# Performance work log

Hardware: AMD Instinct MI355X
Metric: run time of the kernel (lower is better)

## Reference

```python
import jax, jax.numpy as jnp
import numpy as np

HEADS = 16
DIM_HEAD = 64
SCALE = DIM_HEAD ** -0.5


def setup_inputs() -> dict:
    key = jax.random.key(0)
    ks = jax.random.split(key, 6)
    d = 1024
    x = jax.random.normal(ks[0], (4, 2048, d), dtype=jnp.float32)
    s = d ** -0.5
    Wq = jax.random.normal(ks[1], (d, d), dtype=jnp.float32) * s
    Wk = jax.random.normal(ks[2], (d, d), dtype=jnp.float32) * s
    Wv = jax.random.normal(ks[3], (d, d), dtype=jnp.float32) * s
    Wo = jax.random.normal(ks[4], (d, d), dtype=jnp.float32) * s
    bo = jnp.zeros((d,), dtype=jnp.float32)
    return {"x": x, "Wq": Wq, "Wk": Wk, "Wv": Wv, "Wo": Wo, "bo": bo}


def reference(x, Wq, Wk, Wv, Wo, bo):
    b, n, _ = x.shape
    h, dh = HEADS, DIM_HEAD
    # projections (bias-free), split heads: b n (h d) -> b h n d
    def split(t):
        return t.reshape(b, n, h, dh).transpose(0, 2, 1, 3)
    q = split(x @ Wq.T)
    k = split(x @ Wk.T)
    v = split(x @ Wv.T)
    # fp32 scores (inputs already fp32; explicit cast mirrors ATTN_PRECISION='fp32')
    sim = jnp.einsum('bhid,bhjd->bhij', q.astype(jnp.float32), k.astype(jnp.float32)) * SCALE
    attn = jax.nn.softmax(sim, axis=-1)
    out = jnp.einsum('bhij,bhjd->bhid', attn, v)
    out = out.transpose(0, 2, 1, 3).reshape(b, n, h * dh)
    return out @ Wo.T + bo
```

## Files before the change

kernel.cpp:

```cpp
#include <hip/hip_runtime.h>

typedef float f32x4 __attribute__((ext_vector_type(4)));
typedef float f32x16 __attribute__((ext_vector_type(16)));
typedef short s16x8 __attribute__((ext_vector_type(8)));
typedef __bf16 bf16x8 __attribute__((ext_vector_type(8)));
typedef unsigned int u32;
typedef unsigned int u32x4 __attribute__((ext_vector_type(4)));
typedef unsigned short u16;

struct __align__(8) us4 { u16 s[4]; };

#define DEVINL static __device__ __forceinline__

DEVINL f32x4 mfma_bf16(s16x8 a, s16x8 b, f32x4 c) {
  return __builtin_amdgcn_mfma_f32_16x16x32_bf16(
      __builtin_bit_cast(bf16x8, a), __builtin_bit_cast(bf16x8, b), c, 0, 0, 0);
}

DEVINL f32x16 mfma32_bf16(s16x8 a, s16x8 b, f32x16 c) {
  return __builtin_amdgcn_mfma_f32_32x32x16_bf16(
      __builtin_bit_cast(bf16x8, a), __builtin_bit_cast(bf16x8, b), c, 0, 0, 0);
}

DEVINL u16 f2bf(float f) {
  __bf16 h = (__bf16)f;
  return __builtin_bit_cast(u16, h);
}

DEVINL u32 pk2(float a, float b) {
  return (u32)f2bf(a) | ((u32)f2bf(b) << 16);
}

DEVINL void pl32swap(u32& a, u32& b) {
  asm volatile("v_permlane32_swap_b32 %0, %1" : "+v"(a), "+v"(b));
}

DEVINL float exp2_fast(float x) {
  float r;
  asm("v_exp_f32 %0, %1" : "=v"(r) : "v"(x));
  return r;
}

#define GLD16(gp, lp)                                                         \
  __builtin_amdgcn_global_load_lds(                                           \
      (const __attribute__((address_space(1))) void*)(gp),                    \
      (__attribute__((address_space(3))) void*)(lp), 16, 0, 0)

#define SCHEDB() __builtin_amdgcn_sched_barrier(0)

#define WAITV(n)                                                              \
  do {                                                                        \
    asm volatile("s_waitcnt vmcnt(" #n ")" ::: "memory");                     \
    SCHEDB();                                                                 \
  } while (0)

#define BARRIER()                                                             \
  do {                                                                        \
    SCHEDB();                                                                 \
    __builtin_amdgcn_s_barrier();                                             \
    SCHEDB();                                                                 \
  } while (0)

#define PIPE_BAR()                                                            \
  do {                                                                        \
    asm volatile("s_waitcnt vmcnt(0)" ::: "memory");                          \
    SCHEDB();                                                                 \
    __builtin_amdgcn_s_barrier();                                             \
    SCHEDB();                                                                 \
  } while (0)

__global__ __launch_bounds__(256) void convert_k(
    const float* __restrict__ x, const float* __restrict__ wq,
    const float* __restrict__ wk, const float* __restrict__ wv,
    const float* __restrict__ wo, u16* __restrict__ xb,
    u16* __restrict__ wqkv, u16* __restrict__ wob) {
  long i = (long)blockIdx.x * 256 + threadIdx.x;
  const float4* s;
  u16* d;
  if (i < 2097152) {
    s = (const float4*)x + i; d = xb + i * 4;
  } else if (i < 2359296) {
    long j = i - 2097152; s = (const float4*)wq + j; d = wqkv + j * 4;
  } else if (i < 2621440) {
    long j = i - 2359296; s = (const float4*)wk + j; d = wqkv + 1048576 + j * 4;
  } else if (i < 2883584) {
    long j = i - 2621440; s = (const float4*)wv + j; d = wqkv + 2097152 + j * 4;
  } else {
    long j = i - 2883584; s = (const float4*)wo + j; d = wob + j * 4;
  }
  float4 v = *s;
  us4 w;
  w.s[0] = f2bf(v.x); w.s[1] = f2bf(v.y); w.s[2] = f2bf(v.z); w.s[3] = f2bf(v.w);
  *(us4*)d = w;
}

template <int MODE>
__global__ __launch_bounds__(256, 2) void gemm_bt(
    const u16* __restrict__ A, const u16* __restrict__ B,
    u16* __restrict__ oq, u16* __restrict__ ok, u16* __restrict__ ovt,
    float* __restrict__ oc, const float* __restrict__ bias) {
  __shared__ __align__(16) u16 lA[128 * 64];
  __shared__ __align__(16) u16 lB[128 * 64];
  const int t = threadIdx.x;
  const int wave = t >> 6, lane = t & 63, g = lane >> 4, c = lane & 15;
  const int bm = blockIdx.y, bn = blockIdx.x;
  const int wr = wave >> 1, wc = wave & 1;
  f32x4 acc[4][4] = {};
  const long arow0 = (long)bm * 128;
  const long brow0 = (long)bn * 128;

  for (int kk = 0; kk < 1024; kk += 64) {
    __syncthreads();
#pragma unroll
    for (int i = 0; i < 4; ++i) {
      int s = i * 256 + t;
      int row = s >> 3, ch = s & 7;
      int gc = (ch ^ (row & 7)) * 8;
      GLD16(A + (arow0 + row) * 1024 + kk + gc, lA + (i * 256 + wave * 64) * 8);
      GLD16(B + (brow0 + row) * 1024 + kk + gc, lB + (i * 256 + wave * 64) * 8);
    }
    __syncthreads();
#pragma unroll
    for (int k2 = 0; k2 < 2; ++k2) {
      s16x8 af[4], bfr[4];
#pragma unroll
      for (int m = 0; m < 4; ++m) {
        int r = wr * 64 + m * 16 + c;
        af[m] = *(const s16x8*)&lA[r * 64 + (((k2 * 4 + g) ^ (r & 7)) * 8)];
      }
#pragma unroll
      for (int n = 0; n < 4; ++n) {
        int r = wc * 64 + n * 16 + c;
        bfr[n] = *(const s16x8*)&lB[r * 64 + (((k2 * 4 + g) ^ (r & 7)) * 8)];
      }
#pragma unroll
      for (int m = 0; m < 4; ++m)
#pragma unroll
        for (int n = 0; n < 4; ++n)
          acc[m][n] = mfma_bf16(af[m], bfr[n], acc[m][n]);
    }
  }

  if (MODE == 0) {
    const float SQ = 0.18033688011112042f;
#pragma unroll
    for (int n = 0; n < 4; ++n) {
      int colb = bn * 128 + wc * 64 + n * 16;
      int tsel = colb >> 10;
      int f = colb & 1023;
      int h = f >> 6, d0 = f & 63;
#pragma unroll
      for (int m = 0; m < 4; ++m) {
        int row = bm * 128 + wr * 64 + m * 16 + g * 4;
        int b = row >> 11, nn = row & 2047;
        if (tsel == 0) {
          long base = ((long)(b * 16 + h) * 2048 + nn) * 64 + d0 + c;
#pragma unroll
          for (int j = 0; j < 4; ++j)
            oq[base + (long)j * 64] = f2bf(acc[m][n][j] * SQ);
        } else if (tsel == 1) {
          long base = ((long)(b * 16 + h) * 2048 + nn) * 64 + d0 + c;
#pragma unroll
          for (int j = 0; j < 4; ++j)
            ok[base + (long)j * 64] = f2bf(acc[m][n][j]);
        } else {
          us4 w;
#pragma unroll
          for (int j = 0; j < 4; ++j) w.s[j] = f2bf(acc[m][n][j]);
          *(us4*)&ovt[((long)(b * 16 + h) * 64 + d0 + c) * 2048 + nn] = w;
        }
      }
    }
  } else {
#pragma unroll
    for (int n = 0; n < 4; ++n) {
      int col = bn * 128 + wc * 64 + n * 16 + c;
      float bv = bias[col];
#pragma unroll
      for (int m = 0; m < 4; ++m) {
        int row = bm * 128 + wr * 64 + m * 16 + g * 4;
#pragma unroll
        for (int j = 0; j < 4; ++j)
          oc[(long)(row + j) * 1024 + col] = acc[m][n][j] + bv;
      }
    }
  }
}

__global__ __launch_bounds__(256, 4) void flash_attn(
    const u16* __restrict__ q, const u16* __restrict__ k,
    const u16* __restrict__ vt, u16* __restrict__ ao) {
  __shared__ __align__(16) u16 lKV[2 * 8192];
  const int t = threadIdx.x;
  const int wave = t >> 6, lane = t & 63;
  const int lc = lane & 31, hi = lane >> 5, x7 = lc & 7;
  const int wg = blockIdx.x;
  const int bh = wg & 63, qt = wg >> 6;

  const u16* kb = k + (long)bh * (2048 * 64);
  const u16* vb = vt + (long)bh * (64 * 2048);

  const int srow = t >> 3, sch = t & 7;
  const int sgc = (sch ^ (srow & 7)) * 8;
  const u16* kp = kb + srow * 64 + sgc;
  const u16* vp = vb + srow * 2048 + sgc;

  auto stageK = [&](u16* lb) {
    GLD16(kp, lb + wave * 512);
    GLD16(kp + 2048, lb + 2048 + wave * 512);
    kp += 4096;
  };
  auto stageV = [&](u16* lb) {
    GLD16(vp, lb + 4096 + wave * 512);
    GLD16(vp + 65536, lb + 6144 + wave * 512);
    vp += 64;
  };

  const u16* qp =
      q + ((long)bh * 2048 + qt * 128 + wave * 32 + lc) * 64 + hi * 8;
  s16x8 bq[4];
#pragma unroll
  for (int kd = 0; kd < 4; ++kd) bq[kd] = *(const s16x8*)(qp + kd * 16);

  float ls = 0.f;
  f32x16 o[2] = {};

  auto qkt = [&](const u16* lb, f32x16 (&st)[2]) {
    __builtin_amdgcn_s_setprio(1);
#pragma unroll
    for (int ks = 0; ks < 2; ++ks)
#pragma unroll
      for (int kd = 0; kd < 4; ++kd) {
        s16x8 ak =
            *(const s16x8*)&lb[(ks * 32 + lc) * 64 + (((kd * 2 + hi) ^ x7) * 8)];
        st[ks] = mfma32_bf16(ak, bq[kd], st[ks]);
      }
    __builtin_amdgcn_s_setprio(0);
  };

  auto softmax = [&](f32x16 (&st)[2]) {
    float ps = 0.f;
#pragma unroll
    for (int ks = 0; ks < 2; ++ks)
#pragma unroll
      for (int i = 0; i < 16; ++i) {
        float p = exp2_fast(st[ks][i]);
        st[ks][i] = p;
        ps += p;
      }
    ps += __shfl_xor(ps, 32);
    ls += ps;
  };

  auto pv = [&](const u16* lb, f32x16 (&st)[2]) {
    __builtin_amdgcn_s_setprio(1);
#pragma unroll
    for (int ks2 = 0; ks2 < 4; ++ks2) {
      const f32x16& P = st[ks2 >> 1];
      const int b0 = (ks2 & 1) * 8;
      u32 A0 = pk2(P[b0 + 0], P[b0 + 1]);
      u32 B0 = pk2(P[b0 + 2], P[b0 + 3]);
      u32 A1 = pk2(P[b0 + 4], P[b0 + 5]);
      u32 B1 = pk2(P[b0 + 6], P[b0 + 7]);
      pl32swap(A0, A1);
      pl32swap(B0, B1);
      u32x4 pw;
      pw[0] = A0; pw[1] = B0; pw[2] = A1; pw[3] = B1;
      s16x8 bp = __builtin_bit_cast(s16x8, pw);
#pragma unroll
      for (int do2 = 0; do2 < 2; ++do2) {
        s16x8 av = *(const s16x8*)&lb[4096 + (do2 * 32 + lc) * 64 +
                                      (((ks2 * 2 + hi) ^ x7) * 8)];
        o[do2] = mfma32_bf16(av, bp, o[do2]);
      }
    }
    __builtin_amdgcn_s_setprio(0);
  };

  u16* buf0 = lKV;
  u16* buf1 = lKV + 8192;

  stageK(buf0);
  stageV(buf0);
#pragma unroll 1
  for (int i = 0; i < 15; ++i) {
    stageK(buf1);
    stageV(buf1);
    {
      f32x16 st[2] = {};
      WAITV(6);
      qkt(buf0, st);
      softmax(st);
      WAITV(4);
      pv(buf0, st);
    }
    BARRIER();
    stageK(buf0);
    stageV(buf0);
    {
      f32x16 st[2] = {};
      WAITV(6);
      qkt(buf1, st);
      softmax(st);
      WAITV(4);
      pv(buf1, st);
    }
    BARRIER();
  }
  stageK(buf1);
  stageV(buf1);
  {
    f32x16 st[2] = {};
    WAITV(6);
    qkt(buf0, st);
    softmax(st);
    WAITV(4);
    pv(buf0, st);
  }
  BARRIER();
  {
    f32x16 st[2] = {};
    WAITV(2);
    qkt(buf1, st);
    softmax(st);
    WAITV(0);
    pv(buf1, st);
  }

  int b = bh >> 4, h = bh & 15;
  u16* ob = ao + ((long)b * 2048 + qt * 128 + wave * 32 + lc) * 1024 + h * 64 +
            hi * 4;
  float inv = 1.0f / ls;
#pragma unroll
  for (int do2 = 0; do2 < 2; ++do2)
#pragma unroll
    for (int tq = 0; tq < 4; ++tq) {
      us4 w;
#pragma unroll
      for (int j = 0; j < 4; ++j) w.s[j] = f2bf(o[do2][tq * 4 + j] * inv);
      *(us4*)&ob[do2 * 32 + tq * 8] = w;
    }
}

extern "C" void kernel_launch(void* const* d_in, const int* in_sizes, int n_in,
                              void* d_out, int out_size, void* d_ws, size_t ws_size,
                              hipStream_t stream) {
  const float* x = (const float*)d_in[0];
  const float* wq = (const float*)d_in[1];
  const float* wk = (const float*)d_in[2];
  const float* wv = (const float*)d_in[3];
  const float* wo = (const float*)d_in[4];
  const float* bo = (const float*)d_in[5];
  char* ws = (char*)d_ws;
  u16* xb   = (u16*)(ws);
  u16* wqkv = (u16*)(ws + (16l << 20));
  u16* wob  = (u16*)(ws + (22l << 20));
  u16* qb   = (u16*)(ws + (24l << 20));
  u16* kbuf = (u16*)(ws + (40l << 20));
  u16* vtb  = (u16*)(ws + (56l << 20));
  u16* aob  = (u16*)(ws + (72l << 20));
  float* out = (float*)d_out;

  convert_k<<<12288, 256, 0, stream>>>(x, wq, wk, wv, wo, xb, wqkv, wob);
  gemm_bt<0><<<dim3(24, 64), 256, 0, stream>>>(xb, wqkv, qb, kbuf, vtb,
                                               nullptr, nullptr);
  flash_attn<<<1024, 256, 0, stream>>>(qb, kbuf, vtb, aob);
  gemm_bt<1><<<dim3(8, 64), 256, 0, stream>>>(aob, wob, nullptr, nullptr,
                                              nullptr, out, bo);
}
```

Before: 174.9 us.

## Double-buffer GEMM LDS tiles and triple-buffer K in flash attention

The projection GEMM now uses two LDS buffers per operand, prefetching the next k-tile while computing the current one with a single barrier per step instead of two. The attention kernel splits K and V into separate LDS rings, three for K and two for V, so K is fetched two tiles ahead. It also drops the mid-iteration waits between QK^T and PV. Both changes aim to hide global-load latency behind MFMA work, at the cost of doubled GEMM LDS use (64KB, which may cut occupancy) and more attention LDS.

```diff
diff --git a/kernel.cpp b/kernel.cpp
--- a/kernel.cpp
+++ b/kernel.cpp
@@ -99,39 +99,40 @@
     const u16* __restrict__ A, const u16* __restrict__ B,
     u16* __restrict__ oq, u16* __restrict__ ok, u16* __restrict__ ovt,
     float* __restrict__ oc, const float* __restrict__ bias) {
-  __shared__ __align__(16) u16 lA[128 * 64];
-  __shared__ __align__(16) u16 lB[128 * 64];
+  __shared__ __align__(16) u16 lA[2][128 * 64];
+  __shared__ __align__(16) u16 lB[2][128 * 64];
   const int t = threadIdx.x;
   const int wave = t >> 6, lane = t & 63, g = lane >> 4, c = lane & 15;
   const int bm = blockIdx.y, bn = blockIdx.x;
   const int wr = wave >> 1, wc = wave & 1;
   f32x4 acc[4][4] = {};
-  const long arow0 = (long)bm * 128;
-  const long brow0 = (long)bn * 128;
-
-  for (int kk = 0; kk < 1024; kk += 64) {
-    __syncthreads();
+
+  const int srow = t >> 3, sch = t & 7;
+  const int sgc = (sch ^ (srow & 7)) * 8;
+  const u16* abase = A + ((long)bm * 128 + srow) * 1024 + sgc;
+  const u16* bbase = B + ((long)bn * 128 + srow) * 1024 + sgc;
+
+  auto stage = [&](int kk, int bi) {
 #pragma unroll
     for (int i = 0; i < 4; ++i) {
-      int s = i * 256 + t;
-      int row = s >> 3, ch = s & 7;
-      int gc = (ch ^ (row & 7)) * 8;
-      GLD16(A + (arow0 + row) * 1024 + kk + gc, lA + (i * 256 + wave * 64) * 8);
-      GLD16(B + (brow0 + row) * 1024 + kk + gc, lB + (i * 256 + wave * 64) * 8);
-    }
-    __syncthreads();
+      GLD16(abase + i * 32 * 1024 + kk, lA[bi] + (i * 256 + wave * 64) * 8);
+      GLD16(bbase + i * 32 * 1024 + kk, lB[bi] + (i * 256 + wave * 64) * 8);
+    }
+  };
+
+  auto compute = [&](int bi) {
 #pragma unroll
     for (int k2 = 0; k2 < 2; ++k2) {
       s16x8 af[4], bfr[4];
 #pragma unroll
       for (int m = 0; m < 4; ++m) {
         int r = wr * 64 + m * 16 + c;
-        af[m] = *(const s16x8*)&lA[r * 64 + (((k2 * 4 + g) ^ (r & 7)) * 8)];
+        af[m] = *(const s16x8*)&lA[bi][r * 64 + (((k2 * 4 + g) ^ (r & 7)) * 8)];
       }
 #pragma unroll
       for (int n = 0; n < 4; ++n) {
         int r = wc * 64 + n * 16 + c;
-        bfr[n] = *(const s16x8*)&lB[r * 64 + (((k2 * 4 + g) ^ (r & 7)) * 8)];
+        bfr[n] = *(const s16x8*)&lB[bi][r * 64 + (((k2 * 4 + g) ^ (r & 7)) * 8)];
       }
 #pragma unroll
       for (int m = 0; m < 4; ++m)
@@ -139,7 +140,17 @@
         for (int n = 0; n < 4; ++n)
           acc[m][n] = mfma_bf16(af[m], bfr[n], acc[m][n]);
     }
-  }
+  };
+
+  stage(0, 0);
+  PIPE_BAR();
+#pragma unroll 2
+  for (int k = 0; k < 15; ++k) {
+    stage((k + 1) * 64, (k + 1) & 1);
+    compute(k & 1);
+    PIPE_BAR();
+  }
+  compute(1);
 
   if (MODE == 0) {
     const float SQ = 0.18033688011112042f;
@@ -190,7 +201,9 @@
 __global__ __launch_bounds__(256, 4) void flash_attn(
     const u16* __restrict__ q, const u16* __restrict__ k,
     const u16* __restrict__ vt, u16* __restrict__ ao) {
-  __shared__ __align__(16) u16 lKV[2 * 8192];
+  __shared__ __align__(16) u16 lds[20480];
+  u16* const Kb[3] = {lds, lds + 4096, lds + 8192};
+  u16* const Vb[2] = {lds + 12288, lds + 16384};
   const int t = threadIdx.x;
   const int wave = t >> 6, lane = t & 63;
   const int lc = lane & 31, hi = lane >> 5, x7 = lc & 7;
@@ -205,14 +218,14 @@
   const u16* kp = kb + srow * 64 + sgc;
   const u16* vp = vb + srow * 2048 + sgc;
 
-  auto stageK = [&](u16* lb) {
-    GLD16(kp, lb + wave * 512);
-    GLD16(kp + 2048, lb + 2048 + wave * 512);
+  auto stageK = [&](u16* kd) {
+    GLD16(kp, kd + wave * 512);
+    GLD16(kp + 2048, kd + 2048 + wave * 512);
     kp += 4096;
   };
-  auto stageV = [&](u16* lb) {
-    GLD16(vp, lb + 4096 + wave * 512);
-    GLD16(vp + 65536, lb + 6144 + wave * 512);
+  auto stageV = [&](u16* vd) {
+    GLD16(vp, vd + wave * 512);
+    GLD16(vp + 65536, vd + 2048 + wave * 512);
     vp += 64;
   };
 
@@ -225,14 +238,14 @@
   float ls = 0.f;
   f32x16 o[2] = {};
 
-  auto qkt = [&](const u16* lb, f32x16 (&st)[2]) {
+  auto qkt = [&](const u16* kB, f32x16 (&st)[2]) {
     __builtin_amdgcn_s_setprio(1);
 #pragma unroll
     for (int ks = 0; ks < 2; ++ks)
 #pragma unroll
       for (int kd = 0; kd < 4; ++kd) {
         s16x8 ak =
-            *(const s16x8*)&lb[(ks * 32 + lc) * 64 + (((kd * 2 + hi) ^ x7) * 8)];
+            *(const s16x8*)&kB[(ks * 32 + lc) * 64 + (((kd * 2 + hi) ^ x7) * 8)];
         st[ks] = mfma32_bf16(ak, bq[kd], st[ks]);
       }
     __builtin_amdgcn_s_setprio(0);
@@ -252,7 +265,7 @@
     ls += ps;
   };
 
-  auto pv = [&](const u16* lb, f32x16 (&st)[2]) {
+  auto pv = [&](const u16* vB, f32x16 (&st)[2]) {
     __builtin_amdgcn_s_setprio(1);
 #pragma unroll
     for (int ks2 = 0; ks2 < 4; ++ks2) {
@@ -269,7 +282,7 @@
       s16x8 bp = __builtin_bit_cast(s16x8, pw);
 #pragma unroll
       for (int do2 = 0; do2 < 2; ++do2) {
-        s16x8 av = *(const s16x8*)&lb[4096 + (do2 * 32 + lc) * 64 +
+        s16x8 av = *(const s16x8*)&vB[(do2 * 32 + lc) * 64 +
                                       (((ks2 * 2 + hi) ^ x7) * 8)];
         o[do2] = mfma32_bf16(av, bp, o[do2]);
       }
@@ -277,54 +290,43 @@
     __builtin_amdgcn_s_setprio(0);
   };
 
-  u16* buf0 = lKV;
-  u16* buf1 = lKV + 8192;
-
-  stageK(buf0);
-  stageV(buf0);
-#pragma unroll 1
-  for (int i = 0; i < 15; ++i) {
-    stageK(buf1);
-    stageV(buf1);
-    {
-      f32x16 st[2] = {};
-      WAITV(6);
-      qkt(buf0, st);
-      softmax(st);
-      WAITV(4);
-      pv(buf0, st);
-    }
+  stageV(Vb[0]);
+  stageK(Kb[0]);
+  stageK(Kb[1]);
+  WAITV(2);
+  BARRIER();
+
+  u16 *kcur = Kb[0], *knext = Kb[1], *kthird = Kb[2];
+  u16 *vcur = Vb[0], *vother = Vb[1];
+
+#pragma unroll 6
+  for (int t2 = 0; t2 < 30; ++t2) {
+    stageV(vother);
+    stageK(kthird);
+    f32x16 st[2] = {};
+    qkt(kcur, st);
+    softmax(st);
+    pv(vcur, st);
+    WAITV(2);
     BARRIER();
-    stageK(buf0);
-    stageV(buf0);
-    {
-      f32x16 st[2] = {};
-      WAITV(6);
-      qkt(buf1, st);
-      softmax(st);
-      WAITV(4);
-      pv(buf1, st);
-    }
+    u16* tmp = kcur;
+    kcur = knext; knext = kthird; kthird = tmp;
+    tmp = vcur; vcur = vother; vother = tmp;
+  }
+  {
+    stageV(vother);
+    f32x16 st[2] = {};
+    qkt(kcur, st);
+    softmax(st);
+    pv(vcur, st);
+    WAITV(0);
     BARRIER();
   }
-  stageK(buf1);
-  stageV(buf1);
   {
     f32x16 st[2] = {};
-    WAITV(6);
-    qkt(buf0, st);
+    qkt(knext, st);
     softmax(st);
-    WAITV(4);
-    pv(buf0, st);
-  }
-  BARRIER();
-  {
-    f32x16 st[2] = {};
-    WAITV(2);
-    qkt(buf1, st);
-    softmax(st);
-    WAITV(0);
-    pv(buf1, st);
+    pv(vother, st);
   }
 
   int b = bh >> 4, h = bh & 15;
```

New measurement: 186.4 us. 6.6% more time.
